# Kernel optimization log

Hardware: AMD Instinct MI355X
Metric: run time of the kernel (lower is better)

The kernel has to match this reference:

```python
import jax, jax.numpy as jnp
import numpy as np

NEG_INF = -1e30  # large negative instead of float('-inf') for fp16/bf16 safety in softmax


def setup_inputs() -> dict:
    key = jax.random.key(0)
    k1, k2, k3, k4 = jax.random.split(key, 4)
    B, T, C, H = 8, 2048, 768, 64
    x = jax.random.normal(k1, (B, T, C), dtype=jnp.float32)
    # nn.Linear(n_embd, head_size, bias=False): y = x @ W.T, W shape (head_size, n_embd)
    s = 1.0 / np.sqrt(C)
    Wk = jax.random.uniform(k2, (H, C), dtype=jnp.float32, minval=-s, maxval=s)
    Wq = jax.random.uniform(k3, (H, C), dtype=jnp.float32, minval=-s, maxval=s)
    Wv = jax.random.uniform(k4, (H, C), dtype=jnp.float32, minval=-s, maxval=s)
    return {"x": x, "Wk": Wk, "Wq": Wq, "Wv": Wv}


def reference(x, Wk, Wq, Wv):
    # x: [B,T,C]; Wk/Wq/Wv: [H,C]
    k = jnp.einsum('btc,hc->bth', x, Wk)  # [B,T,H]
    q = jnp.einsum('btc,hc->bth', x, Wq)
    v = jnp.einsum('btc,hc->bth', x, Wv)
    att = jnp.einsum('bqh,bkh->bqk', q, k)  # [B,T,T], NOTE: no 1/sqrt(H) scaling, faithful to source
    T = x.shape[1]
    causal = jnp.tril(jnp.ones((T, T), dtype=bool))
    att = jnp.where(causal, att, NEG_INF)
    att = jax.nn.softmax(att, axis=-1)
    out = jnp.einsum('bqk,bkh->bqh', att, v)  # [B,T,H]
    return out
```

## Files before the change

kernel.cpp:

```cpp
#include <hip/hip_runtime.h>
#include <hip/hip_bf16.h>
#include <stdint.h>

typedef float    f32x4  __attribute__((ext_vector_type(4)));
typedef float    f32x16 __attribute__((ext_vector_type(16)));
typedef short    s16x8  __attribute__((ext_vector_type(8)));
typedef uint32_t u32x4  __attribute__((ext_vector_type(4)));

#define NB 8
#define NT 2048
#define NC 768
#define NH 64
#define LOG2E 1.4426950408889634f

__device__ __forceinline__ uint32_t f2bf1(float f) {
  union { float f; uint32_t u; } v; v.f = f;
  uint32_t u = v.u;
  return (u + 0x7fffu + ((u >> 16) & 1u)) >> 16;
}
__device__ __forceinline__ uint32_t packbf2(float lo, float hi) {
  union { __hip_bfloat162 h; uint32_t u; } c;
  c.h = __float22bfloat162_rn(float2{lo, hi});
  return c.u;
}

__global__ __launch_bounds__(256) void wconv_kernel(
    const float* __restrict__ Wk, const float* __restrict__ Wq,
    const float* __restrict__ Wv, short* __restrict__ Wb)
{
  int idx = blockIdx.x * 256 + threadIdx.x;
  if (idx >= 192 * 768) return;
  int n = idx / 768;
  float v;
  if (n < 64)       v = Wq[idx];
  else if (n < 128) v = Wk[idx - 64 * 768];
  else              v = Wv[idx - 128 * 768];
  Wb[idx] = (short)f2bf1(v);
}

__global__ __launch_bounds__(512, 2) void proj_kernel(
    const float* __restrict__ x, const short* __restrict__ Wb,
    short* __restrict__ qf_buf, short* __restrict__ kf_buf, short* __restrict__ vf_buf)
{
  __shared__ float slots[4 * 3072];
  short* ldsQT = (short*)slots;
  short* ldsKT = (short*)slots + 2176;
  short* ldsVT = (short*)slots + 4352;

  const int tid  = threadIdx.x;
  const int lane = tid & 63;
  const int w    = tid >> 6;
  const int kh   = w >> 1;
  const int nh   = w & 1;
  const int col  = lane & 31;
  const int half = lane >> 5;
  const int t0   = blockIdx.x * 32;

  const float* xsrc = x + (size_t)(t0 + col) * NC + kh * 192 + half * 8;
  const short* w0 = Wb + (size_t)((nh * 3 + 0) * 32 + col) * NC + kh * 192 + half * 8;
  const short* w1 = w0 + 32 * NC;
  const short* w2 = w1 + 32 * NC;

  f32x16 acc[3];
#pragma unroll
  for (int j = 0; j < 3; ++j)
#pragma unroll
    for (int e = 0; e < 16; ++e) acc[j][e] = 0.f;

  f32x4 xA[2], xB[2];
  s16x8 wA[3], wB[3];
  auto loadS = [&](f32x4* xr, s16x8* wr, int ks) {
    xr[0] = *(const f32x4*)(xsrc + ks * 16);
    xr[1] = *(const f32x4*)(xsrc + ks * 16 + 4);
    wr[0] = *(const s16x8*)(w0 + ks * 16);
    wr[1] = *(const s16x8*)(w1 + ks * 16);
    wr[2] = *(const s16x8*)(w2 + ks * 16);
  };
  auto computeS = [&](f32x4* xr, s16x8* wr) {
    union { u32x4 u; s16x8 v; } af;
    af.u = (u32x4){packbf2(xr[0][0], xr[0][1]), packbf2(xr[0][2], xr[0][3]),
                   packbf2(xr[1][0], xr[1][1]), packbf2(xr[1][2], xr[1][3])};
    acc[0] = __builtin_amdgcn_mfma_f32_32x32x16_bf16(af.v, wr[0], acc[0], 0, 0, 0);
    acc[1] = __builtin_amdgcn_mfma_f32_32x32x16_bf16(af.v, wr[1], acc[1], 0, 0, 0);
    acc[2] = __builtin_amdgcn_mfma_f32_32x32x16_bf16(af.v, wr[2], acc[2], 0, 0, 0);
  };

  loadS(xA, wA, 0);
#pragma unroll
  for (int ks = 0; ks < 12; ks += 2) {
    loadS(xB, wB, ks + 1);
    computeS(xA, wA);
    if (ks + 2 < 12) loadS(xA, wA, ks + 2);
    computeS(xB, wB);
  }

  if (kh >= 2) {
    float* sl = slots + ((kh - 2) * 2 + nh) * 3072;
#pragma unroll
    for (int j = 0; j < 3; ++j)
#pragma unroll
      for (int r = 0; r < 16; ++r) {
        int rd = (r & 3) + 8 * (r >> 2) + 4 * half;
        sl[rd * 96 + j * 32 + col] = acc[j][r];
      }
  }
  __syncthreads();
  if (kh < 2) {
    float* sl = slots + (kh * 2 + nh) * 3072;
#pragma unroll
    for (int j = 0; j < 3; ++j)
#pragma unroll
      for (int r = 0; r < 16; ++r) {
        int rd = (r & 3) + 8 * (r >> 2) + 4 * half;
        acc[j][r] += sl[rd * 96 + j * 32 + col];
      }
  }
  __syncthreads();
  if (kh == 1) {
    float* sl = slots + (2 + nh) * 3072;
#pragma unroll
    for (int j = 0; j < 3; ++j)
#pragma unroll
      for (int r = 0; r < 16; ++r) {
        int rd = (r & 3) + 8 * (r >> 2) + 4 * half;
        sl[rd * 96 + j * 32 + col] = acc[j][r];
      }
  }
  __syncthreads();
  if (kh == 0) {
    float* sl = slots + (2 + nh) * 3072;
#pragma unroll
    for (int j = 0; j < 3; ++j)
#pragma unroll
      for (int r = 0; r < 16; ++r) {
        int rd = (r & 3) + 8 * (r >> 2) + 4 * half;
        float sum = acc[j][r] + sl[rd * 96 + j * 32 + col];
        int nn = nh * 96 + j * 32 + col;
        if (nn < 64)        ldsQT[rd * 68 + nn]        = (short)f2bf1(sum * LOG2E);
        else if (nn < 128)  ldsKT[rd * 68 + (nn - 64)] = (short)f2bf1(sum);
        else                ldsVT[(nn - 128) * 34 + rd] = (short)f2bf1(sum);
      }
  }
  __syncthreads();

  {
    const int b  = t0 >> 11;
    const int kt = (t0 >> 5) & 63;
    const size_t base = ((size_t)(b * 64 + kt) * 4) * 512;
    if (w < 4) {
      s16x8 vq = *(const s16x8*)&ldsQT[col * 68 + w * 16 + half * 8];
      *(s16x8*)&qf_buf[base + w * 512 + lane * 8] = vq;
      s16x8 vk = *(const s16x8*)&ldsKT[col * 68 + w * 16 + half * 8];
      *(s16x8*)&kf_buf[base + w * 512 + lane * 8] = vk;
    } else {
      int i = w - 4;
      s16x8 vv = *(const s16x8*)&ldsVT[(col + (i >> 1) * 32) * 34 + (i & 1) * 16 + half * 8];
      *(s16x8*)&vf_buf[base + i * 512 + lane * 8] = vv;
    }
  }
}

__global__ __launch_bounds__(256, 2) void attn_kernel(
    const short* __restrict__ qf_buf, const short* __restrict__ kf_buf,
    const short* __restrict__ vf_buf, float* __restrict__ out)
{
  __shared__ float ldsO[4][32][65];
  __shared__ float ldsM[4][32];
  __shared__ float ldsL[4][32];

  const int tid  = threadIdx.x;
  const int lane = tid & 63;
  const int w    = tid >> 6;
  const int col  = lane & 31;
  const int half = lane >> 5;
  const int b    = blockIdx.x >> 6;
  int qt = blockIdx.x & 63;
  if (blockIdx.x & 256) qt = 63 - qt;
  const int q0 = qt * 32;
  const int nT = qt + 1;
  const int tBeg = (w * nT) >> 2;
  const int tEnd = ((w + 1) * nT) >> 2;

  s16x8 qf[4];
  {
    const short* qp = qf_buf + ((size_t)(b * 64 + qt) * 4) * 512 + lane * 8;
#pragma unroll
    for (int ks = 0; ks < 4; ++ks) qf[ks] = *(const s16x8*)(qp + ks * 512);
  }
  const short* kfb = kf_buf + (size_t)b * 64 * 2048 + lane * 8;
  const short* vfb = vf_buf + (size_t)b * 64 * 2048 + lane * 8;

  f32x16 oacc[2];
#pragma unroll
  for (int i = 0; i < 2; ++i)
#pragma unroll
    for (int e = 0; e < 16; ++e) oacc[i][e] = 0.f;
  float m = -1e30f, l = 0.f;

  s16x8 kA[4], vA[4], kB[4], vB[4];
  auto loadT = [&](s16x8* dk, s16x8* dv, int t) {
    const short* kp = kfb + (size_t)t * 2048;
    const short* vp = vfb + (size_t)t * 2048;
#pragma unroll
    for (int i = 0; i < 4; ++i) {
      dk[i] = *(const s16x8*)(kp + i * 512);
      dv[i] = *(const s16x8*)(vp + i * 512);
    }
  };
  auto body = [&](s16x8* ck, s16x8* cv, int t) {
    f32x16 s;
#pragma unroll
    for (int e = 0; e < 16; ++e) s[e] = 0.f;
#pragma unroll
    for (int ks = 0; ks < 4; ++ks)
      s = __builtin_amdgcn_mfma_f32_32x32x16_bf16(ck[ks], qf[ks], s, 0, 0, 0);

    if (t == nT - 1) {
#pragma unroll
      for (int r = 0; r < 16; ++r) {
        int rd = (r & 3) + 8 * (r >> 2) + 4 * half;
        if (rd > col) s[r] = -1e30f;
      }
    }
    float vmax = s[0];
#pragma unroll
    for (int r = 1; r < 16; ++r) vmax = fmaxf(vmax, s[r]);
    vmax = fmaxf(vmax, __shfl_xor(vmax, 32));
    float mn    = fmaxf(m, vmax);
    float alpha = exp2f(m - mn);
    float p[16];
    float rs = 0.f;
#pragma unroll
    for (int r = 0; r < 16; ++r) { p[r] = exp2f(s[r] - mn); rs += p[r]; }
    rs += __shfl_xor(rs, 32);
    l = l * alpha + rs;
    m = mn;
#pragma unroll
    for (int i = 0; i < 2; ++i)
#pragma unroll
      for (int e = 0; e < 16; ++e) oacc[i][e] *= alpha;

    uint32_t pw[8];
#pragma unroll
    for (int i = 0; i < 8; ++i) pw[i] = packbf2(p[2 * i], p[2 * i + 1]);
#pragma unroll
    for (int kc = 0; kc < 2; ++kc) {
      uint32_t s0 = half ? pw[4 * kc]     : pw[4 * kc + 2];
      uint32_t s1 = half ? pw[4 * kc + 1] : pw[4 * kc + 3];
      uint32_t r0 = __shfl_xor(s0, 32);
      uint32_t r1 = __shfl_xor(s1, 32);
      uint32_t w0 = half ? r0 : pw[4 * kc];
      uint32_t w1 = half ? r1 : pw[4 * kc + 1];
      uint32_t w2 = half ? pw[4 * kc + 2] : r0;
      uint32_t w3 = half ? pw[4 * kc + 3] : r1;
      union { u32x4 u; s16x8 v; } pf;
      pf.u = (u32x4){w0, w1, w2, w3};
#pragma unroll
      for (int ht = 0; ht < 2; ++ht)
        oacc[ht] = __builtin_amdgcn_mfma_f32_32x32x16_bf16(cv[ht * 2 + kc], pf.v, oacc[ht], 0, 0, 0);
    }
  };

  int t = tBeg;
  if (t < tEnd) loadT(kA, vA, t);
  if (t + 1 < tEnd) loadT(kB, vB, t + 1);
  for (; t + 1 < tEnd; t += 2) {
    body(kA, vA, t);
    if (t + 2 < tEnd) loadT(kA, vA, t + 2);
    body(kB, vB, t + 1);
    if (t + 3 < tEnd) loadT(kB, vB, t + 3);
  }
  if (t < tEnd) body(kA, vA, t);

  if (half == 0) { ldsM[w][col] = m; ldsL[w][col] = l; }
#pragma unroll
  for (int ht = 0; ht < 2; ++ht)
#pragma unroll
    for (int r = 0; r < 16; ++r) {
      int rd = (r & 3) + 8 * (r >> 2) + 4 * half;
      ldsO[w][col][ht * 32 + rd] = oacc[ht][r];
    }
  __syncthreads();

  const int q  = tid >> 3;
  const int h0 = (tid & 7) * 8;
  float mv[4], lv[4];
#pragma unroll
  for (int i = 0; i < 4; ++i) { mv[i] = ldsM[i][q]; lv[i] = ldsL[i][q]; }
  float M = fmaxf(fmaxf(mv[0], mv[1]), fmaxf(mv[2], mv[3]));
  float cf[4], L = 0.f;
#pragma unroll
  for (int i = 0; i < 4; ++i) { cf[i] = exp2f(mv[i] - M); L += cf[i] * lv[i]; }
  float inv = 1.0f / L;
  float o[8];
#pragma unroll
  for (int j = 0; j < 8; ++j) {
    float a = 0.f;
#pragma unroll
    for (int i = 0; i < 4; ++i) a += cf[i] * ldsO[i][q][h0 + j];
    o[j] = a * inv;
  }
  float* obase = out + (size_t)(b * NT + q0 + q) * NH + h0;
  *(f32x4*)obase       = (f32x4){o[0], o[1], o[2], o[3]};
  *(f32x4*)(obase + 4) = (f32x4){o[4], o[5], o[6], o[7]};
}

extern "C" void kernel_launch(void* const* d_in, const int* in_sizes, int n_in,
                              void* d_out, int out_size, void* d_ws, size_t ws_size,
                              hipStream_t stream) {
  const float* x  = (const float*)d_in[0];
  const float* Wk = (const float*)d_in[1];
  const float* Wq = (const float*)d_in[2];
  const float* Wv = (const float*)d_in[3];
  float* out = (float*)d_out;

  char* ws = (char*)d_ws;
  short* Wb  = (short*)(ws);
  short* qfb = (short*)(ws + (512 << 10));
  short* kfb = (short*)(ws + (512 << 10) + (2 << 20));
  short* vfb = (short*)(ws + (512 << 10) + (4 << 20));

  hipLaunchKernelGGL(wconv_kernel, dim3(576), dim3(256), 0, stream, Wk, Wq, Wv, Wb);
  hipLaunchKernelGGL(proj_kernel,  dim3(512), dim3(512), 0, stream, x, Wb, qfb, kfb, vfb);
  hipLaunchKernelGGL(attn_kernel,  dim3(512), dim3(256), 0, stream, qfb, kfb, vfb, out);
}
```

Baseline: 133.4 us.

## Restructure projection and attention kernels with prepacked weights and paired query tiles

Weights are now prepacked into MFMA fragment order, with the log2e scale folded into Wq. The projection kernel stages x as bf16 in swizzled LDS, uses 4 waves that each cover all 192 outputs over a K slice, and reduces the partials in LDS. The attention kernel now launches 512-thread blocks that each pair a short and a long causal query tile, split the 8 waves between them in proportion to their work, and merge partial outputs stored as bf16 in LDS. This aims to balance causal work and cut global weight traffic, at the cost of extra bf16 rounding on the partial outputs and a heavier LDS footprint.

```diff
diff --git a/kernel.cpp b/kernel.cpp
--- a/kernel.cpp
+++ b/kernel.cpp
@@ -6,6 +6,7 @@
 typedef float    f32x16 __attribute__((ext_vector_type(16)));
 typedef short    s16x8  __attribute__((ext_vector_type(8)));
 typedef uint32_t u32x4  __attribute__((ext_vector_type(4)));
+typedef uint32_t u32x2  __attribute__((ext_vector_type(2)));
 
 #define NB 8
 #define NT 2048
@@ -23,167 +24,192 @@
   c.h = __float22bfloat162_rn(float2{lo, hi});
   return c.u;
 }
+__device__ __forceinline__ float bf2f(short s) {
+  union { float f; uint32_t u; } v; v.u = ((uint32_t)(uint16_t)s) << 16; return v.f;
+}
 
 __global__ __launch_bounds__(256) void wconv_kernel(
     const float* __restrict__ Wk, const float* __restrict__ Wq,
-    const float* __restrict__ Wv, short* __restrict__ Wb)
+    const float* __restrict__ Wv, short* __restrict__ Wf)
 {
-  int idx = blockIdx.x * 256 + threadIdx.x;
-  if (idx >= 192 * 768) return;
-  int n = idx / 768;
-  float v;
-  if (n < 64)       v = Wq[idx];
-  else if (n < 128) v = Wk[idx - 64 * 768];
-  else              v = Wv[idx - 128 * 768];
-  Wb[idx] = (short)f2bf1(v);
-}
-
-__global__ __launch_bounds__(512, 2) void proj_kernel(
-    const float* __restrict__ x, const short* __restrict__ Wb,
+  int f = blockIdx.x * 256 + threadIdx.x;
+  int lane = f & 63;
+  int rest = f >> 6;
+  int ks = rest % 48;
+  int nt = rest / 48;
+  int col = lane & 31, half = lane >> 5;
+  int n = nt * 32 + col;
+  int k = ks * 16 + half * 8;
+  const float* src;
+  float sc = 1.0f;
+  if (n < 64)       { src = Wq + (size_t)n * NC + k; sc = LOG2E; }
+  else if (n < 128) { src = Wk + (size_t)(n - 64) * NC + k; }
+  else              { src = Wv + (size_t)(n - 128) * NC + k; }
+  f32x4 a = *(const f32x4*)src;
+  f32x4 b = *(const f32x4*)(src + 4);
+  u32x4 o = {packbf2(a[0] * sc, a[1] * sc), packbf2(a[2] * sc, a[3] * sc),
+             packbf2(b[0] * sc, b[1] * sc), packbf2(b[2] * sc, b[3] * sc)};
+  *(u32x4*)&Wf[(size_t)f * 8] = o;
+}
+
+__global__ __launch_bounds__(256, 2) void proj_kernel(
+    const float* __restrict__ x, const short* __restrict__ Wf,
     short* __restrict__ qf_buf, short* __restrict__ kf_buf, short* __restrict__ vf_buf)
 {
-  __shared__ float slots[4 * 3072];
-  short* ldsQT = (short*)slots;
-  short* ldsKT = (short*)slots + 2176;
-  short* ldsVT = (short*)slots + 4352;
-
-  const int tid  = threadIdx.x;
-  const int lane = tid & 63;
-  const int w    = tid >> 6;
-  const int kh   = w >> 1;
-  const int nh   = w & 1;
-  const int col  = lane & 31;
-  const int half = lane >> 5;
-  const int t0   = blockIdx.x * 32;
-
-  const float* xsrc = x + (size_t)(t0 + col) * NC + kh * 192 + half * 8;
-  const short* w0 = Wb + (size_t)((nh * 3 + 0) * 32 + col) * NC + kh * 192 + half * 8;
-  const short* w1 = w0 + 32 * NC;
-  const short* w2 = w1 + 32 * NC;
-
-  f32x16 acc[3];
-#pragma unroll
-  for (int j = 0; j < 3; ++j)
-#pragma unroll
-    for (int e = 0; e < 16; ++e) acc[j][e] = 0.f;
-
-  f32x4 xA[2], xB[2];
-  s16x8 wA[3], wB[3];
-  auto loadS = [&](f32x4* xr, s16x8* wr, int ks) {
-    xr[0] = *(const f32x4*)(xsrc + ks * 16);
-    xr[1] = *(const f32x4*)(xsrc + ks * 16 + 4);
-    wr[0] = *(const s16x8*)(w0 + ks * 16);
-    wr[1] = *(const s16x8*)(w1 + ks * 16);
-    wr[2] = *(const s16x8*)(w2 + ks * 16);
-  };
-  auto computeS = [&](f32x4* xr, s16x8* wr) {
-    union { u32x4 u; s16x8 v; } af;
-    af.u = (u32x4){packbf2(xr[0][0], xr[0][1]), packbf2(xr[0][2], xr[0][3]),
-                   packbf2(xr[1][0], xr[1][1]), packbf2(xr[1][2], xr[1][3])};
-    acc[0] = __builtin_amdgcn_mfma_f32_32x32x16_bf16(af.v, wr[0], acc[0], 0, 0, 0);
-    acc[1] = __builtin_amdgcn_mfma_f32_32x32x16_bf16(af.v, wr[1], acc[1], 0, 0, 0);
-    acc[2] = __builtin_amdgcn_mfma_f32_32x32x16_bf16(af.v, wr[2], acc[2], 0, 0, 0);
-  };
-
-  loadS(xA, wA, 0);
-#pragma unroll
-  for (int ks = 0; ks < 12; ks += 2) {
-    loadS(xB, wB, ks + 1);
-    computeS(xA, wA);
-    if (ks + 2 < 12) loadS(xA, wA, ks + 2);
-    computeS(xB, wB);
-  }
-
-  if (kh >= 2) {
-    float* sl = slots + ((kh - 2) * 2 + nh) * 3072;
-#pragma unroll
-    for (int j = 0; j < 3; ++j)
-#pragma unroll
-      for (int r = 0; r < 16; ++r) {
-        int rd = (r & 3) + 8 * (r >> 2) + 4 * half;
-        sl[rd * 96 + j * 32 + col] = acc[j][r];
-      }
-  }
-  __syncthreads();
-  if (kh < 2) {
-    float* sl = slots + (kh * 2 + nh) * 3072;
-#pragma unroll
-    for (int j = 0; j < 3; ++j)
-#pragma unroll
-      for (int r = 0; r < 16; ++r) {
-        int rd = (r & 3) + 8 * (r >> 2) + 4 * half;
-        acc[j][r] += sl[rd * 96 + j * 32 + col];
-      }
-  }
-  __syncthreads();
-  if (kh == 1) {
-    float* sl = slots + (2 + nh) * 3072;
-#pragma unroll
-    for (int j = 0; j < 3; ++j)
-#pragma unroll
-      for (int r = 0; r < 16; ++r) {
-        int rd = (r & 3) + 8 * (r >> 2) + 4 * half;
-        sl[rd * 96 + j * 32 + col] = acc[j][r];
-      }
-  }
-  __syncthreads();
-  if (kh == 0) {
-    float* sl = slots + (2 + nh) * 3072;
-#pragma unroll
-    for (int j = 0; j < 3; ++j)
-#pragma unroll
-      for (int r = 0; r < 16; ++r) {
-        int rd = (r & 3) + 8 * (r >> 2) + 4 * half;
-        float sum = acc[j][r] + sl[rd * 96 + j * 32 + col];
-        int nn = nh * 96 + j * 32 + col;
-        if (nn < 64)        ldsQT[rd * 68 + nn]        = (short)f2bf1(sum * LOG2E);
-        else if (nn < 128)  ldsKT[rd * 68 + (nn - 64)] = (short)f2bf1(sum);
-        else                ldsVT[(nn - 128) * 34 + rd] = (short)f2bf1(sum);
-      }
-  }
-  __syncthreads();
-
-  {
-    const int b  = t0 >> 11;
-    const int kt = (t0 >> 5) & 63;
-    const size_t base = ((size_t)(b * 64 + kt) * 4) * 512;
-    if (w < 4) {
-      s16x8 vq = *(const s16x8*)&ldsQT[col * 68 + w * 16 + half * 8];
-      *(s16x8*)&qf_buf[base + w * 512 + lane * 8] = vq;
-      s16x8 vk = *(const s16x8*)&ldsKT[col * 68 + w * 16 + half * 8];
-      *(s16x8*)&kf_buf[base + w * 512 + lane * 8] = vk;
-    } else {
-      int i = w - 4;
-      s16x8 vv = *(const s16x8*)&ldsVT[(col + (i >> 1) * 32) * 34 + (i & 1) * 16 + half * 8];
-      *(s16x8*)&vf_buf[base + i * 512 + lane * 8] = vv;
-    }
-  }
-}
-
-__global__ __launch_bounds__(256, 2) void attn_kernel(
-    const short* __restrict__ qf_buf, const short* __restrict__ kf_buf,
-    const short* __restrict__ vf_buf, float* __restrict__ out)
-{
-  __shared__ float ldsO[4][32][65];
-  __shared__ float ldsM[4][32];
-  __shared__ float ldsL[4][32];
+  __shared__ char smem[49152];
+  short* ldsX  = (short*)smem;
+  float* slot0 = (float*)smem;
+  float* slot1 = (float*)(smem + 24576);
+  short* ldsQT = (short*)(smem + 24576);
+  short* ldsKT = ldsQT + 2176;
+  short* ldsVT = ldsQT + 4352;
 
   const int tid  = threadIdx.x;
   const int lane = tid & 63;
   const int w    = tid >> 6;
   const int col  = lane & 31;
   const int half = lane >> 5;
-  const int b    = blockIdx.x >> 6;
-  int qt = blockIdx.x & 63;
-  if (blockIdx.x & 256) qt = 63 - qt;
-  const int q0 = qt * 32;
-  const int nT = qt + 1;
-  const int tBeg = (w * nT) >> 2;
-  const int tEnd = ((w + 1) * nT) >> 2;
+  const int t0   = blockIdx.x * 32;
+
+  {
+    const int tok = tid >> 3, g = tid & 7;
+    const float* src = x + (size_t)(t0 + tok) * NC + g * 8;
+    short* drow = ldsX + tok * 768;
+#pragma unroll
+    for (int i = 0; i < 12; ++i) {
+      f32x4 a = *(const f32x4*)(src + i * 64);
+      f32x4 b = *(const f32x4*)(src + i * 64 + 4);
+      int grp = g + i * 8;
+      int swz = (grp & ~7) | ((grp ^ tok) & 7);
+      u32x4 o = {packbf2(a[0], a[1]), packbf2(a[2], a[3]),
+                 packbf2(b[0], b[1]), packbf2(b[2], b[3])};
+      *(u32x4*)&drow[swz * 8] = o;
+    }
+  }
+  __syncthreads();
+
+  f32x16 acc[6];
+#pragma unroll
+  for (int j = 0; j < 6; ++j)
+#pragma unroll
+    for (int e = 0; e < 16; ++e) acc[j][e] = 0.f;
+
+  const short* wbase = Wf + lane * 8;
+  auto loadW = [&](s16x8* d, int ks) {
+#pragma unroll
+    for (int nt = 0; nt < 6; ++nt)
+      d[nt] = *(const s16x8*)(wbase + ((size_t)(nt * 48 + ks) << 9));
+  };
+  auto loadA = [&](int ks) -> s16x8 {
+    int grp = ks * 2 + half;
+    int swz = (grp & ~7) | ((grp ^ col) & 7);
+    return *(const s16x8*)&ldsX[col * 768 + swz * 8];
+  };
+
+  {
+    const int ks0 = w * 12;
+    s16x8 wA[6], wB[6], aA, aB;
+    loadW(wA, ks0);
+    aA = loadA(ks0);
+#pragma unroll
+    for (int s = 0; s < 12; s += 2) {
+      loadW(wB, ks0 + s + 1);
+      aB = loadA(ks0 + s + 1);
+#pragma unroll
+      for (int nt = 0; nt < 6; ++nt)
+        acc[nt] = __builtin_amdgcn_mfma_f32_32x32x16_bf16(aA, wA[nt], acc[nt], 0, 0, 0);
+      if (s + 2 < 12) { loadW(wA, ks0 + s + 2); aA = loadA(ks0 + s + 2); }
+#pragma unroll
+      for (int nt = 0; nt < 6; ++nt)
+        acc[nt] = __builtin_amdgcn_mfma_f32_32x32x16_bf16(aB, wB[nt], acc[nt], 0, 0, 0);
+    }
+  }
+
+  auto putSlot = [&](float* sl) {
+#pragma unroll
+    for (int nt = 0; nt < 6; ++nt)
+#pragma unroll
+      for (int r = 0; r < 16; ++r) {
+        int rd = (r & 3) + 8 * (r >> 2) + 4 * half;
+        sl[rd * 192 + nt * 32 + col] = acc[nt][r];
+      }
+  };
+  auto addSlot = [&](float* sl) {
+#pragma unroll
+    for (int nt = 0; nt < 6; ++nt)
+#pragma unroll
+      for (int r = 0; r < 16; ++r) {
+        int rd = (r & 3) + 8 * (r >> 2) + 4 * half;
+        acc[nt][r] += sl[rd * 192 + nt * 32 + col];
+      }
+  };
+
+  __syncthreads();
+  if (w >= 2) putSlot(w == 2 ? slot0 : slot1);
+  __syncthreads();
+  if (w < 2) addSlot(w == 0 ? slot0 : slot1);
+  __syncthreads();
+  if (w == 1) putSlot(slot0);
+  __syncthreads();
+  if (w == 0) {
+    addSlot(slot0);
+#pragma unroll
+    for (int nt = 0; nt < 6; ++nt) {
+      int n = nt * 32 + col;
+#pragma unroll
+      for (int r = 0; r < 16; ++r) {
+        int rd = (r & 3) + 8 * (r >> 2) + 4 * half;
+        short v = (short)f2bf1(acc[nt][r]);
+        if (n < 64)       ldsQT[rd * 68 + n] = v;
+        else if (n < 128) ldsKT[rd * 68 + (n - 64)] = v;
+        else              ldsVT[(n - 128) * 34 + rd] = v;
+      }
+    }
+  }
+  __syncthreads();
+
+  {
+    const int b  = t0 >> 11;
+    const int kt = (t0 >> 5) & 63;
+    const size_t base = (size_t)(b * 64 + kt) * 2048;
+    s16x8 vq = *(const s16x8*)&ldsQT[col * 68 + w * 16 + half * 8];
+    *(s16x8*)&qf_buf[base + w * 512 + lane * 8] = vq;
+    s16x8 vk = *(const s16x8*)&ldsKT[col * 68 + w * 16 + half * 8];
+    *(s16x8*)&kf_buf[base + w * 512 + lane * 8] = vk;
+    s16x8 vv = *(const s16x8*)&ldsVT[(col + (w >> 1) * 32) * 34 + (w & 1) * 16 + half * 8];
+    *(s16x8*)&vf_buf[base + w * 512 + lane * 8] = vv;
+  }
+}
+
+__global__ __launch_bounds__(512, 2) void attn_kernel(
+    const short* __restrict__ qf_buf, const short* __restrict__ kf_buf,
+    const short* __restrict__ vf_buf, float* __restrict__ out)
+{
+  __shared__ short ldsOb[8][32][72];
+  __shared__ float ldsM[8][32];
+  __shared__ float ldsL[8][32];
+
+  const int tid  = threadIdx.x;
+  const int lane = tid & 63;
+  const int w    = tid >> 6;
+  const int col  = lane & 31;
+  const int half = lane >> 5;
+  const int b    = blockIdx.x & 7;
+  const int pr   = blockIdx.x >> 3;
+  const int qtL = pr, qtH = 63 - pr;
+  const int Hn = 64 - pr, Ln = pr + 1;
+  int nH = (8 * Hn + 32) / 65;
+  if (nH < 1) nH = 1;
+  if (nH > 7) nH = 7;
+  const int nL = 8 - nH;
+
+  int qt, tBeg, tEnd;
+  if (w < nH) { qt = qtH; tBeg = (w * Hn) / nH; tEnd = ((w + 1) * Hn) / nH; }
+  else        { int wl = w - nH; qt = qtL; tBeg = (wl * Ln) / nL; tEnd = ((wl + 1) * Ln) / nL; }
 
   s16x8 qf[4];
   {
-    const short* qp = qf_buf + ((size_t)(b * 64 + qt) * 4) * 512 + lane * 8;
+    const short* qp = qf_buf + (size_t)(b * 64 + qt) * 2048 + lane * 8;
 #pragma unroll
     for (int ks = 0; ks < 4; ++ks) qf[ks] = *(const s16x8*)(qp + ks * 512);
   }
@@ -215,7 +241,7 @@
     for (int ks = 0; ks < 4; ++ks)
       s = __builtin_amdgcn_mfma_f32_32x32x16_bf16(ck[ks], qf[ks], s, 0, 0, 0);
 
-    if (t == nT - 1) {
+    if (t == qt) {
 #pragma unroll
       for (int r = 0; r < 16; ++r) {
         int rd = (r & 3) + 8 * (r >> 2) + 4 * half;
@@ -276,33 +302,39 @@
 #pragma unroll
   for (int ht = 0; ht < 2; ++ht)
 #pragma unroll
-    for (int r = 0; r < 16; ++r) {
-      int rd = (r & 3) + 8 * (r >> 2) + 4 * half;
-      ldsO[w][col][ht * 32 + rd] = oacc[ht][r];
-    }
-  __syncthreads();
-
-  const int q  = tid >> 3;
-  const int h0 = (tid & 7) * 8;
-  float mv[4], lv[4];
-#pragma unroll
-  for (int i = 0; i < 4; ++i) { mv[i] = ldsM[i][q]; lv[i] = ldsL[i][q]; }
-  float M = fmaxf(fmaxf(mv[0], mv[1]), fmaxf(mv[2], mv[3]));
-  float cf[4], L = 0.f;
-#pragma unroll
-  for (int i = 0; i < 4; ++i) { cf[i] = exp2f(mv[i] - M); L += cf[i] * lv[i]; }
-  float inv = 1.0f / L;
-  float o[8];
-#pragma unroll
-  for (int j = 0; j < 8; ++j) {
-    float a = 0.f;
-#pragma unroll
-    for (int i = 0; i < 4; ++i) a += cf[i] * ldsO[i][q][h0 + j];
-    o[j] = a * inv;
-  }
-  float* obase = out + (size_t)(b * NT + q0 + q) * NH + h0;
-  *(f32x4*)obase       = (f32x4){o[0], o[1], o[2], o[3]};
-  *(f32x4*)(obase + 4) = (f32x4){o[4], o[5], o[6], o[7]};
+    for (int u = 0; u < 4; ++u) {
+      int h = ht * 32 + 8 * u + 4 * half;
+      u32x2 pk = {packbf2(oacc[ht][4 * u + 0], oacc[ht][4 * u + 1]),
+                  packbf2(oacc[ht][4 * u + 2], oacc[ht][4 * u + 3])};
+      *(u32x2*)&ldsOb[w][col][h] = pk;
+    }
+  __syncthreads();
+
+  {
+    const int seg = tid >> 8;
+    const int rr  = (tid >> 3) & 31;
+    const int h0  = (tid & 7) * 8;
+    const int s0  = seg ? nH : 0;
+    const int s1  = seg ? 8 : nH;
+    float M = -1e30f;
+    for (int s = s0; s < s1; ++s) M = fmaxf(M, ldsM[s][rr]);
+    float Ls = 0.f;
+    float o[8];
+#pragma unroll
+    for (int j = 0; j < 8; ++j) o[j] = 0.f;
+    for (int s = s0; s < s1; ++s) {
+      float cf = exp2f(ldsM[s][rr] - M);
+      Ls += cf * ldsL[s][rr];
+      s16x8 raw = *(const s16x8*)&ldsOb[s][rr][h0];
+#pragma unroll
+      for (int j = 0; j < 8; ++j) o[j] += cf * bf2f(raw[j]);
+    }
+    float inv = 1.0f / Ls;
+    int qrow = (seg ? qtL : qtH) * 32 + rr;
+    float* ob = out + (size_t)(b * NT + qrow) * NH + h0;
+    *(f32x4*)ob       = (f32x4){o[0] * inv, o[1] * inv, o[2] * inv, o[3] * inv};
+    *(f32x4*)(ob + 4) = (f32x4){o[4] * inv, o[5] * inv, o[6] * inv, o[7] * inv};
+  }
 }
 
 extern "C" void kernel_launch(void* const* d_in, const int* in_sizes, int n_in,
@@ -315,12 +347,12 @@
   float* out = (float*)d_out;
 
   char* ws = (char*)d_ws;
-  short* Wb  = (short*)(ws);
+  short* Wf  = (short*)(ws);
   short* qfb = (short*)(ws + (512 << 10));
   short* kfb = (short*)(ws + (512 << 10) + (2 << 20));
   short* vfb = (short*)(ws + (512 << 10) + (4 << 20));
 
-  hipLaunchKernelGGL(wconv_kernel, dim3(576), dim3(256), 0, stream, Wk, Wq, Wv, Wb);
-  hipLaunchKernelGGL(proj_kernel,  dim3(512), dim3(512), 0, stream, x, Wb, qfb, kfb, vfb);
-  hipLaunchKernelGGL(attn_kernel,  dim3(512), dim3(256), 0, stream, qfb, kfb, vfb, out);
-}
+  hipLaunchKernelGGL(wconv_kernel, dim3(72),  dim3(256), 0, stream, Wk, Wq, Wv, Wf);
+  hipLaunchKernelGGL(proj_kernel,  dim3(512), dim3(256), 0, stream, x, Wf, qfb, kfb, vfb);
+  hipLaunchKernelGGL(attn_kernel,  dim3(256), dim3(512), 0, stream, qfb, kfb, vfb, out);
+}
```

New measurement: 115.6 us. 1.15x faster.
